# Kernel tuning notes

Hardware: AMD Instinct MI355X
Metric: run time of the kernel (lower is better)

## Reference

```python
import jax, jax.numpy as jnp
import numpy as np

B, S, H, NH = 1, 4096, 1024, 16
HD = H // NH  # head_dim = 64
ROPE_BASE = 10000.0


def setup_inputs() -> dict:
    key = jax.random.key(0)
    ks = jax.random.split(key, 8)
    sc = 0.02
    return {
        "hidden_states": jax.random.normal(ks[0], (B, S, H), jnp.float32),
        "attention_mask": jnp.zeros((B, 1, 1, S), jnp.float32),
        "Wq": jax.random.normal(ks[1], (H, H), jnp.float32) * sc,
        "bq": jnp.zeros((H,), jnp.float32),
        "Wk": jax.random.normal(ks[2], (H, H), jnp.float32) * sc,
        "bk": jnp.zeros((H,), jnp.float32),
        "Wv": jax.random.normal(ks[3], (H, H), jnp.float32) * sc,
        "bv": jnp.zeros((H,), jnp.float32),
    }


def _rope_tables(seq_len, head_dim, dtype):
    inv_freq = 1.0 / (ROPE_BASE ** (jnp.arange(0, head_dim, 2, dtype=jnp.float32) / head_dim))
    t = jnp.arange(seq_len, dtype=jnp.float32)
    freqs = jnp.einsum("s,d->sd", t, inv_freq)          # [S, HD/2]
    emb = jnp.concatenate([freqs, freqs], axis=-1)       # [S, HD]
    return jnp.cos(emb).astype(dtype), jnp.sin(emb).astype(dtype)


def _rotate_half(x):
    x1, x2 = jnp.split(x, 2, axis=-1)
    return jnp.concatenate([-x2, x1], axis=-1)


def reference(hidden_states, attention_mask, Wq, bq, Wk, bk, Wv, bv):
    bsz, q_len, _ = hidden_states.shape
    # QKV projections (torch Linear: x @ W.T + b), split into heads -> [B, NH, S, HD]
    def heads(x):
        return x.reshape(bsz, q_len, NH, HD).transpose(0, 2, 1, 3)
    q = heads(hidden_states @ Wq.T + bq)
    k = heads(hidden_states @ Wk.T + bk)
    v = heads(hidden_states @ Wv.T + bv)

    # RoPE with position_ids = arange(kv_seq_len)
    cos, sin = _rope_tables(q_len, HD, q.dtype)          # [S, HD]
    cos = cos[None, None]                                 # [1,1,S,HD]
    sin = sin[None, None]
    q = q * cos + _rotate_half(q) * sin
    k = k * cos + _rotate_half(k) * sin

    # Manual scaled-dot-product attention (baddbmm + softmax + matmul)
    scale = HD ** (-0.5)
    scores = jnp.einsum("bhqd,bhkd->bhqk", q, k) * scale  # [B,NH,S,S]
    scores = scores + attention_mask                      # broadcast additive mask
    weights = jax.nn.softmax(scores, axis=-1)
    attn = jnp.einsum("bhqk,bhkd->bhqd", weights, v)      # [B,NH,S,HD]

    # [B,S,NH,HD] -> [B,S,H]
    return attn.transpose(0, 2, 1, 3).reshape(bsz, q_len, NH * HD)
```

## Files before the change

kernel.cpp:

```cpp
#include <hip/hip_runtime.h>
#include <hip/hip_bf16.h>
#include <math.h>
#include <stdint.h>

#define S_ 4096
#define H_ 1024
#define NH_ 16
#define HD_ 64
#define LOG2E 1.4426950408889634f
#define QSCALE (0.125f * LOG2E)

typedef __bf16 bf16;
typedef __attribute__((ext_vector_type(8))) __bf16 bf16x8;
typedef __attribute__((ext_vector_type(4))) __bf16 bf16x4;
typedef __attribute__((ext_vector_type(4))) float f32x4;
typedef __attribute__((ext_vector_type(16))) float f32x16;
typedef __attribute__((ext_vector_type(2))) float f32x2;
typedef __attribute__((ext_vector_type(2))) int int2v;

__device__ __forceinline__ f32x4 mfma16(bf16x8 a, bf16x8 b, f32x4 c) {
    return __builtin_amdgcn_mfma_f32_16x16x32_bf16(a, b, c, 0, 0, 0);
}
__device__ __forceinline__ f32x16 mfma32(bf16x8 a, bf16x8 b, f32x16 c) {
    return __builtin_amdgcn_mfma_f32_32x32x16_bf16(a, b, c, 0, 0, 0);
}

__device__ __forceinline__ void gload16(const void* g, void* l) {
    __builtin_amdgcn_global_load_lds(
        (__attribute__((address_space(1))) void*)(uintptr_t)g,
        (__attribute__((address_space(3))) void*)(uintptr_t)l,
        16, 0, 0);
}

__device__ __forceinline__ unsigned cvtpk(float a, float b) {
    unsigned r;
    asm("v_cvt_pk_bf16_f32 %0, %1, %2" : "=v"(r) : "v"(a), "v"(b));
    return r;
}

__device__ __forceinline__ void swap32(unsigned a, unsigned b, unsigned& r0, unsigned& r1) {
#if __has_builtin(__builtin_amdgcn_permlane32_swap)
    int2v rr = __builtin_amdgcn_permlane32_swap((int)a, (int)b, false, false);
    r0 = (unsigned)rr[0];
    r1 = (unsigned)rr[1];
#else
    unsigned sa = (unsigned)__shfl_xor((int)a, 32, 64);
    unsigned sb = (unsigned)__shfl_xor((int)b, 32, 64);
    bool hi = (threadIdx.x & 32) != 0;
    r0 = hi ? sb : a;
    r1 = hi ? b : sa;
#endif
}

__device__ __forceinline__ float fexp2(float x) {
#if __has_builtin(__builtin_amdgcn_exp2f)
    return __builtin_amdgcn_exp2f(x);
#else
    return exp2f(x);
#endif
}

__global__ __launch_bounds__(256) void cvt_kernel(const float* __restrict__ src,
                                                  bf16* __restrict__ dst, int n) {
    int i = (blockIdx.x * 256 + threadIdx.x) * 8;
    if (i >= n) return;
    float4 v0 = *reinterpret_cast<const float4*>(src + i);
    float4 v1 = *reinterpret_cast<const float4*>(src + i + 4);
    bf16x8 o;
    o[0] = (bf16)v0.x; o[1] = (bf16)v0.y; o[2] = (bf16)v0.z; o[3] = (bf16)v0.w;
    o[4] = (bf16)v1.x; o[5] = (bf16)v1.y; o[6] = (bf16)v1.z; o[7] = (bf16)v1.w;
    *reinterpret_cast<bf16x8*>(dst + i) = o;
}

__global__ __launch_bounds__(256) void rope_table_kernel(float2* __restrict__ tab) {
    int idx = blockIdx.x * 256 + threadIdx.x;
    if (idx >= S_ * 32) return;
    int i = idx & 31, s = idx >> 5;
    double ang = (double)s * exp(-(double)(2 * i) / 64.0 * log(10000.0));
    tab[idx] = make_float2((float)cos(ang), (float)sin(ang));
}

__global__ __launch_bounds__(256) void maskl_kernel(const float* __restrict__ mask,
                                                    float* __restrict__ maskL) {
    int i = blockIdx.x * 256 + threadIdx.x;
    if (i < S_) maskL[i] = mask[i] * LOG2E;
}

__global__ __launch_bounds__(256) void qkv_gemm_kernel(
    const bf16* __restrict__ Xb,
    const bf16* __restrict__ Wqb, const bf16* __restrict__ Wkb, const bf16* __restrict__ Wvb,
    const float* __restrict__ bqp, const float* __restrict__ bkp, const float* __restrict__ bvp,
    const float2* __restrict__ tab,
    bf16* __restrict__ Qo, bf16* __restrict__ Ko, bf16* __restrict__ Vto)
{
    __shared__ bf16 Alds[128 * 64];
    __shared__ bf16 Blds[128 * 64];
    const int z = blockIdx.z;
    const bf16* W = z == 0 ? Wqb : z == 1 ? Wkb : Wvb;
    const float* bias = z == 0 ? bqp : z == 1 ? bkp : bvp;
    const int tm = blockIdx.y * 128, tn = blockIdx.x * 128;
    const int tid = threadIdx.x, lane = tid & 63, wid = tid >> 6;
    const int wm = (wid >> 1) * 64, wn = (wid & 1) * 64;
    const int lr = lane & 15, lg = lane >> 4;
    const int c_row = tid >> 3, c_sub = tid & 7;

    f32x4 acc[4][4] = {};

    for (int kt = 0; kt < H_; kt += 64) {
        #pragma unroll
        for (int is = 0; is < 4; ++is) {
            int row = is * 32 + c_row;
            int sub = c_sub ^ (row & 7);
            gload16(&Xb[(size_t)(tm + row) * H_ + kt + sub * 8],
                    &Alds[(is * 256 + wid * 64) * 8]);
            gload16(&W[(size_t)(tn + row) * H_ + kt + sub * 8],
                    &Blds[(is * 256 + wid * 64) * 8]);
        }
        __syncthreads();

        #pragma unroll
        for (int kc = 0; kc < 2; ++kc) {
            bf16x8 af[4], bfr[4];
            #pragma unroll
            for (int mb = 0; mb < 4; ++mb) {
                int row = wm + mb * 16 + lr;
                int ch = (kc * 4 + lg) ^ (row & 7);
                af[mb] = *reinterpret_cast<const bf16x8*>(&Alds[row * 64 + ch * 8]);
            }
            #pragma unroll
            for (int nb = 0; nb < 4; ++nb) {
                int row = wn + nb * 16 + lr;
                int ch = (kc * 4 + lg) ^ (row & 7);
                bfr[nb] = *reinterpret_cast<const bf16x8*>(&Blds[row * 64 + ch * 8]);
            }
            #pragma unroll
            for (int mb = 0; mb < 4; ++mb)
                #pragma unroll
                for (int nb = 0; nb < 4; ++nb)
                    acc[mb][nb] = mfma16(af[mb], bfr[nb], acc[mb][nb]);
        }
        __syncthreads();
    }

    float bv4[4];
    #pragma unroll
    for (int nb = 0; nb < 4; ++nb) bv4[nb] = bias[tn + wn + nb * 16 + lr];

    if (z < 2) {
        bf16* Y = z == 0 ? Qo : Ko;
        const float fs = z == 0 ? QSCALE : 1.0f;
        #pragma unroll
        for (int mb = 0; mb < 4; ++mb) {
            #pragma unroll
            for (int r = 0; r < 4; ++r) {
                int row = tm + wm + mb * 16 + lg * 4 + r;
                #pragma unroll
                for (int nb = 0; nb < 2; ++nb) {
                    float2 cs = tab[row * 32 + nb * 16 + lr];
                    float x1 = acc[mb][nb][r] + bv4[nb];
                    float x2 = acc[mb][nb + 2][r] + bv4[nb + 2];
                    int col = tn + wn + nb * 16 + lr;
                    Y[(size_t)row * H_ + col]      = (bf16)((x1 * cs.x - x2 * cs.y) * fs);
                    Y[(size_t)row * H_ + col + 32] = (bf16)((x2 * cs.x + x1 * cs.y) * fs);
                }
            }
        }
    } else {
        #pragma unroll
        for (int mb = 0; mb < 4; ++mb) {
            int rowb = tm + wm + mb * 16 + lg * 4;
            #pragma unroll
            for (int nb = 0; nb < 4; ++nb) {
                int col = tn + wn + nb * 16 + lr;
                bf16x4 pk;
                #pragma unroll
                for (int r = 0; r < 4; ++r) pk[r] = (bf16)(acc[mb][nb][r] + bv4[nb]);
                *reinterpret_cast<bf16x4*>(&Vto[(size_t)col * S_ + rowb]) = pk;
            }
        }
    }
}

__global__ __launch_bounds__(256) void attn_kernel(
    const bf16* __restrict__ Q, const bf16* __restrict__ K, const bf16* __restrict__ Vt,
    const float* __restrict__ maskL, float* __restrict__ out)
{
    __shared__ bf16 Kl[2][64 * 64];
    __shared__ bf16 Vl[3][64 * 64];
    const int h = blockIdx.y;
    const int qb = blockIdx.x * 128;
    const int tid = threadIdx.x, lane = tid & 63, wid = tid >> 6;
    const int l31 = lane & 31, hi = lane >> 5;
    const int srow = wid * 8 + (lane >> 3);
    const int ssub = (lane & 7) ^ (srow & 7);

    bf16x8 qf[4];
    {
        const bf16* qp = &Q[(size_t)(qb + wid * 32 + l31) * H_ + h * 64 + hi * 8];
        #pragma unroll
        for (int ks = 0; ks < 4; ++ks)
            qf[ks] = *reinterpret_cast<const bf16x8*>(qp + ks * 16);
    }

    bf16x8 vones;
    #pragma unroll
    for (int j = 0; j < 8; ++j) vones[j] = (bf16)1.0f;

    f32x16 o0 = {}, o1 = {}, lacc = {};

    const bf16* kg = &K[(size_t)srow * H_ + h * 64 + ssub * 8];
    const bf16* vg = &Vt[(size_t)(h * 64 + srow) * S_ + ssub * 8];

    auto STAGE_K = [&](int buf) {
        gload16(kg,           &Kl[buf][(wid * 8) * 64]);
        gload16(kg + 32 * H_, &Kl[buf][(32 + wid * 8) * 64]);
        kg += 64 * H_;
    };
    auto STAGE_V = [&](int buf) {
        gload16(vg,           &Vl[buf][(wid * 8) * 64]);
        gload16(vg + 32 * S_, &Vl[buf][(32 + wid * 8) * 64]);
        vg += 64;
    };

    auto QK = [&](const bf16* Kb_, const float* mrow, f32x16& q0, f32x16& q1) {
        f32x16 a, b;
        #pragma unroll
        for (int g = 0; g < 4; ++g) {
            float4 m0 = *reinterpret_cast<const float4*>(mrow + g * 8);
            a[g * 4 + 0] = m0.x; a[g * 4 + 1] = m0.y;
            a[g * 4 + 2] = m0.z; a[g * 4 + 3] = m0.w;
            float4 m1 = *reinterpret_cast<const float4*>(mrow + 32 + g * 8);
            b[g * 4 + 0] = m1.x; b[g * 4 + 1] = m1.y;
            b[g * 4 + 2] = m1.z; b[g * 4 + 3] = m1.w;
        }
        __builtin_amdgcn_s_setprio(1);
        #pragma unroll
        for (int ks = 0; ks < 4; ++ks) {
            int ch = (2 * ks + hi) ^ (l31 & 7);
            bf16x8 kf0 = *reinterpret_cast<const bf16x8*>(&Kb_[l31 * 64 + ch * 8]);
            a = mfma32(kf0, qf[ks], a);
            bf16x8 kf1 = *reinterpret_cast<const bf16x8*>(&Kb_[(32 + l31) * 64 + ch * 8]);
            b = mfma32(kf1, qf[ks], b);
        }
        __builtin_amdgcn_s_setprio(0);
        q0 = a; q1 = b;
    };

    STAGE_K(0); STAGE_V(0);
    STAGE_K(1); STAGE_V(1);
    __syncthreads();

    f32x16 scA0, scA1, scB0, scB1;
    QK(Kl[0], &maskL[hi * 4], scA0, scA1);

    int vstage = 2;
    int vread = 0;
    const float* mlp = &maskL[64 + hi * 4];
    const int NT = S_ / 64;

    auto BODY = [&](int t, f32x16& sm0, f32x16& sm1, f32x16& qk0, f32x16& qk1) {
        __syncthreads();
        if (t + 1 < NT) { QK(Kl[(t + 1) & 1], mlp, qk0, qk1); mlp += 64; }
        if (t + 2 < NT) {
            STAGE_K(t & 1);
            STAGE_V(vstage);
            vstage = vstage == 2 ? 0 : vstage + 1;
        }

        #pragma unroll
        for (int r = 0; r < 16; ++r) sm0[r] = fexp2(sm0[r]);
        #pragma unroll
        for (int r = 0; r < 16; ++r) sm1[r] = fexp2(sm1[r]);

        bf16x8 pf[4];
        #pragma unroll
        for (int ks = 0; ks < 2; ++ks) {
            unsigned w[4];
            #pragma unroll
            for (int wi = 0; wi < 2; ++wi) {
                unsigned u = cvtpk(sm0[8 * ks + 2 * wi],     sm0[8 * ks + 2 * wi + 1]);
                unsigned v = cvtpk(sm0[8 * ks + 4 + 2 * wi], sm0[8 * ks + 4 + 2 * wi + 1]);
                swap32(u, v, w[wi], w[wi + 2]);
            }
            union { unsigned u[4]; bf16x8 v; } cv;
            cv.u[0] = w[0]; cv.u[1] = w[1]; cv.u[2] = w[2]; cv.u[3] = w[3];
            pf[ks] = cv.v;
        }
        #pragma unroll
        for (int ks = 0; ks < 2; ++ks) {
            unsigned w[4];
            #pragma unroll
            for (int wi = 0; wi < 2; ++wi) {
                unsigned u = cvtpk(sm1[8 * ks + 2 * wi],     sm1[8 * ks + 2 * wi + 1]);
                unsigned v = cvtpk(sm1[8 * ks + 4 + 2 * wi], sm1[8 * ks + 4 + 2 * wi + 1]);
                swap32(u, v, w[wi], w[wi + 2]);
            }
            union { unsigned u[4]; bf16x8 v; } cv;
            cv.u[0] = w[0]; cv.u[1] = w[1]; cv.u[2] = w[2]; cv.u[3] = w[3];
            pf[2 + ks] = cv.v;
        }

        const bf16* Vb_ = Vl[vread];
        __builtin_amdgcn_s_setprio(1);
        #pragma unroll
        for (int ks = 0; ks < 4; ++ks) {
            int ch = (2 * ks + hi) ^ (l31 & 7);
            bf16x8 vf0 = *reinterpret_cast<const bf16x8*>(&Vb_[l31 * 64 + ch * 8]);
            o0 = mfma32(vf0, pf[ks], o0);
            bf16x8 vf1 = *reinterpret_cast<const bf16x8*>(&Vb_[(32 + l31) * 64 + ch * 8]);
            o1 = mfma32(vf1, pf[ks], o1);
            lacc = mfma32(vones, pf[ks], lacc);
        }
        __builtin_amdgcn_s_setprio(0);
        vread = vread == 2 ? 0 : vread + 1;
    };

    for (int t = 0; t < NT; t += 2) {
        BODY(t,     scA0, scA1, scB0, scB1);
        BODY(t + 1, scB0, scB1, scA0, scA1);
    }

    float inv = 1.f / lacc[0];
    float* orow = &out[(size_t)(qb + wid * 32 + l31) * H_ + h * 64];
    #pragma unroll
    for (int g2 = 0; g2 < 4; ++g2) {
        float4 a, b;
        a.x = o0[g2 * 4 + 0] * inv; a.y = o0[g2 * 4 + 1] * inv;
        a.z = o0[g2 * 4 + 2] * inv; a.w = o0[g2 * 4 + 3] * inv;
        b.x = o1[g2 * 4 + 0] * inv; b.y = o1[g2 * 4 + 1] * inv;
        b.z = o1[g2 * 4 + 2] * inv; b.w = o1[g2 * 4 + 3] * inv;
        *reinterpret_cast<float4*>(orow + 8 * g2 + 4 * hi) = a;
        *reinterpret_cast<float4*>(orow + 32 + 8 * g2 + 4 * hi) = b;
    }
}

extern "C" void kernel_launch(void* const* d_in, const int* in_sizes, int n_in,
                              void* d_out, int out_size, void* d_ws, size_t ws_size,
                              hipStream_t stream) {
    const float* hs   = (const float*)d_in[0];
    const float* mask = (const float*)d_in[1];
    const float* Wq   = (const float*)d_in[2];
    const float* bq   = (const float*)d_in[3];
    const float* Wk   = (const float*)d_in[4];
    const float* bk   = (const float*)d_in[5];
    const float* Wv   = (const float*)d_in[6];
    const float* bv   = (const float*)d_in[7];
    float* out = (float*)d_out;

    char* ws = (char*)d_ws;
    bf16* Xb    = (bf16*)(ws);
    bf16* Wqb   = (bf16*)(ws + (8u  << 20));
    bf16* Wkb   = (bf16*)(ws + (10u << 20));
    bf16* Wvb   = (bf16*)(ws + (12u << 20));
    bf16* Qb    = (bf16*)(ws + (14u << 20));
    bf16* Kb    = (bf16*)(ws + (22u << 20));
    bf16* Vt    = (bf16*)(ws + (30u << 20));
    float2* tab = (float2*)(ws + (38u << 20));
    float* maskL = (float*)(ws + (39u << 20));

    cvt_kernel<<<S_ * H_ / 2048, 256, 0, stream>>>(hs, Xb, S_ * H_);
    cvt_kernel<<<H_ * H_ / 2048, 256, 0, stream>>>(Wq, Wqb, H_ * H_);
    cvt_kernel<<<H_ * H_ / 2048, 256, 0, stream>>>(Wk, Wkb, H_ * H_);
    cvt_kernel<<<H_ * H_ / 2048, 256, 0, stream>>>(Wv, Wvb, H_ * H_);
    rope_table_kernel<<<(S_ * 32) / 256, 256, 0, stream>>>(tab);
    maskl_kernel<<<(S_ + 255) / 256, 256, 0, stream>>>(mask, maskL);
    qkv_gemm_kernel<<<dim3(H_ / 128, S_ / 128, 3), 256, 0, stream>>>(
        Xb, Wqb, Wkb, Wvb, bq, bk, bv, tab, Qb, Kb, Vt);
    attn_kernel<<<dim3(S_ / 128, NH_), 256, 0, stream>>>(Qb, Kb, Vt, maskL, out);
}
```

Baseline: 164.2 us.

## Fold additive mask into V and row-sum weights; merge prep launches

The additive attention mask is turned into a multiplicative weight exp(mask). That weight scales the V rows in the QKV GEMM epilogue and replaces the all-ones operand in the row-sum MFMA, so the QK accumulators start from zero instead of loading mask values every tile. The four conversion launches are merged into one kernel, and the rope-table and mask preprocessing are merged into a single prep kernel, cutting launch overhead. In exchange, the row-sum MFMA now reads a bf16 weight vector from global memory each tile. Rounding exp(mask) to bf16 can change precision, and the scheme depends on exp(mask) staying finite.

Measured after the change: 152.9 us. 1.07x faster.

```diff
diff --git a/kernel.cpp b/kernel.cpp
--- a/kernel.cpp
+++ b/kernel.cpp
@@ -60,10 +60,18 @@
 #endif
 }
 
-__global__ __launch_bounds__(256) void cvt_kernel(const float* __restrict__ src,
-                                                  bf16* __restrict__ dst, int n) {
-    int i = (blockIdx.x * 256 + threadIdx.x) * 8;
-    if (i >= n) return;
+__global__ __launch_bounds__(256) void cvt_all_kernel(
+    const float* __restrict__ hs, const float* __restrict__ Wq,
+    const float* __restrict__ Wk, const float* __restrict__ Wv,
+    bf16* __restrict__ Xb, bf16* __restrict__ Wqb,
+    bf16* __restrict__ Wkb, bf16* __restrict__ Wvb) {
+    int b = blockIdx.x;
+    const float* src; bf16* dst; size_t base;
+    if (b < 2048)      { src = hs; dst = Xb;  base = (size_t)b * 2048; }
+    else if (b < 2560) { src = Wq; dst = Wqb; base = (size_t)(b - 2048) * 2048; }
+    else if (b < 3072) { src = Wk; dst = Wkb; base = (size_t)(b - 2560) * 2048; }
+    else               { src = Wv; dst = Wvb; base = (size_t)(b - 3072) * 2048; }
+    size_t i = base + threadIdx.x * 8;
     float4 v0 = *reinterpret_cast<const float4*>(src + i);
     float4 v1 = *reinterpret_cast<const float4*>(src + i + 4);
     bf16x8 o;
@@ -72,25 +80,29 @@
     *reinterpret_cast<bf16x8*>(dst + i) = o;
 }
 
-__global__ __launch_bounds__(256) void rope_table_kernel(float2* __restrict__ tab) {
+__global__ __launch_bounds__(256) void prep_kernel(const float* __restrict__ mask,
+                                                   float2* __restrict__ tab,
+                                                   bf16* __restrict__ wM,
+                                                   float* __restrict__ wV) {
     int idx = blockIdx.x * 256 + threadIdx.x;
-    if (idx >= S_ * 32) return;
-    int i = idx & 31, s = idx >> 5;
-    double ang = (double)s * exp(-(double)(2 * i) / 64.0 * log(10000.0));
-    tab[idx] = make_float2((float)cos(ang), (float)sin(ang));
-}
-
-__global__ __launch_bounds__(256) void maskl_kernel(const float* __restrict__ mask,
-                                                    float* __restrict__ maskL) {
-    int i = blockIdx.x * 256 + threadIdx.x;
-    if (i < S_) maskL[i] = mask[i] * LOG2E;
+    if (idx < S_ * 32) {
+        int i = idx & 31, s = idx >> 5;
+        double ang = (double)s * exp(-(double)(2 * i) / 64.0 * log(10000.0));
+        tab[idx] = make_float2((float)cos(ang), (float)sin(ang));
+    }
+    if (idx < S_) {
+        float e = exp2f(mask[idx] * LOG2E);
+        bf16 eb = (bf16)e;
+        wM[idx] = eb;
+        wV[idx] = (float)eb;
+    }
 }
 
 __global__ __launch_bounds__(256) void qkv_gemm_kernel(
     const bf16* __restrict__ Xb,
     const bf16* __restrict__ Wqb, const bf16* __restrict__ Wkb, const bf16* __restrict__ Wvb,
     const float* __restrict__ bqp, const float* __restrict__ bkp, const float* __restrict__ bvp,
-    const float2* __restrict__ tab,
+    const float2* __restrict__ tab, const float* __restrict__ wV,
     bf16* __restrict__ Qo, bf16* __restrict__ Ko, bf16* __restrict__ Vto)
 {
     __shared__ bf16 Alds[128 * 64];
@@ -169,12 +181,15 @@
         #pragma unroll
         for (int mb = 0; mb < 4; ++mb) {
             int rowb = tm + wm + mb * 16 + lg * 4;
+            float4 wv = *reinterpret_cast<const float4*>(&wV[rowb]);
+            float wvr[4] = {wv.x, wv.y, wv.z, wv.w};
             #pragma unroll
             for (int nb = 0; nb < 4; ++nb) {
                 int col = tn + wn + nb * 16 + lr;
                 bf16x4 pk;
                 #pragma unroll
-                for (int r = 0; r < 4; ++r) pk[r] = (bf16)(acc[mb][nb][r] + bv4[nb]);
+                for (int r = 0; r < 4; ++r)
+                    pk[r] = (bf16)((acc[mb][nb][r] + bv4[nb]) * wvr[r]);
                 *reinterpret_cast<bf16x4*>(&Vto[(size_t)col * S_ + rowb]) = pk;
             }
         }
@@ -183,7 +198,7 @@
 
 __global__ __launch_bounds__(256) void attn_kernel(
     const bf16* __restrict__ Q, const bf16* __restrict__ K, const bf16* __restrict__ Vt,
-    const float* __restrict__ maskL, float* __restrict__ out)
+    const bf16* __restrict__ wM, float* __restrict__ out)
 {
     __shared__ bf16 Kl[2][64 * 64];
     __shared__ bf16 Vl[3][64 * 64];
@@ -201,10 +216,6 @@
         for (int ks = 0; ks < 4; ++ks)
             qf[ks] = *reinterpret_cast<const bf16x8*>(qp + ks * 16);
     }
-
-    bf16x8 vones;
-    #pragma unroll
-    for (int j = 0; j < 8; ++j) vones[j] = (bf16)1.0f;
 
     f32x16 o0 = {}, o1 = {}, lacc = {};
 
@@ -222,17 +233,8 @@
         vg += 64;
     };
 
-    auto QK = [&](const bf16* Kb_, const float* mrow, f32x16& q0, f32x16& q1) {
-        f32x16 a, b;
-        #pragma unroll
-        for (int g = 0; g < 4; ++g) {
-            float4 m0 = *reinterpret_cast<const float4*>(mrow + g * 8);
-            a[g * 4 + 0] = m0.x; a[g * 4 + 1] = m0.y;
-            a[g * 4 + 2] = m0.z; a[g * 4 + 3] = m0.w;
-            float4 m1 = *reinterpret_cast<const float4*>(mrow + 32 + g * 8);
-            b[g * 4 + 0] = m1.x; b[g * 4 + 1] = m1.y;
-            b[g * 4 + 2] = m1.z; b[g * 4 + 3] = m1.w;
-        }
+    auto QK = [&](const bf16* Kb_, f32x16& q0, f32x16& q1) {
+        f32x16 a = {}, b = {};
         __builtin_amdgcn_s_setprio(1);
         #pragma unroll
         for (int ks = 0; ks < 4; ++ks) {
@@ -251,16 +253,16 @@
     __syncthreads();
 
     f32x16 scA0, scA1, scB0, scB1;
-    QK(Kl[0], &maskL[hi * 4], scA0, scA1);
+    QK(Kl[0], scA0, scA1);
 
     int vstage = 2;
     int vread = 0;
-    const float* mlp = &maskL[64 + hi * 4];
+    const bf16* wmt = wM + hi * 8;
     const int NT = S_ / 64;
 
     auto BODY = [&](int t, f32x16& sm0, f32x16& sm1, f32x16& qk0, f32x16& qk1) {
         __syncthreads();
-        if (t + 1 < NT) { QK(Kl[(t + 1) & 1], mlp, qk0, qk1); mlp += 64; }
+        if (t + 1 < NT) QK(Kl[(t + 1) & 1], qk0, qk1);
         if (t + 2 < NT) {
             STAGE_K(t & 1);
             STAGE_V(vstage);
@@ -309,9 +311,11 @@
             o0 = mfma32(vf0, pf[ks], o0);
             bf16x8 vf1 = *reinterpret_cast<const bf16x8*>(&Vb_[(32 + l31) * 64 + ch * 8]);
             o1 = mfma32(vf1, pf[ks], o1);
-            lacc = mfma32(vones, pf[ks], lacc);
+            bf16x8 wf = *reinterpret_cast<const bf16x8*>(wmt + ks * 16);
+            lacc = mfma32(wf, pf[ks], lacc);
         }
         __builtin_amdgcn_s_setprio(0);
+        wmt += 64;
         vread = vread == 2 ? 0 : vread + 1;
     };
 
@@ -356,15 +360,12 @@
     bf16* Kb    = (bf16*)(ws + (22u << 20));
     bf16* Vt    = (bf16*)(ws + (30u << 20));
     float2* tab = (float2*)(ws + (38u << 20));
-    float* maskL = (float*)(ws + (39u << 20));
-
-    cvt_kernel<<<S_ * H_ / 2048, 256, 0, stream>>>(hs, Xb, S_ * H_);
-    cvt_kernel<<<H_ * H_ / 2048, 256, 0, stream>>>(Wq, Wqb, H_ * H_);
-    cvt_kernel<<<H_ * H_ / 2048, 256, 0, stream>>>(Wk, Wkb, H_ * H_);
-    cvt_kernel<<<H_ * H_ / 2048, 256, 0, stream>>>(Wv, Wvb, H_ * H_);
-    rope_table_kernel<<<(S_ * 32) / 256, 256, 0, stream>>>(tab);
-    maskl_kernel<<<(S_ + 255) / 256, 256, 0, stream>>>(mask, maskL);
+    bf16* wM    = (bf16*)(ws + (39u << 20));
+    float* wV   = (float*)(ws + (39u << 20) + 65536);
+
+    cvt_all_kernel<<<3584, 256, 0, stream>>>(hs, Wq, Wk, Wv, Xb, Wqb, Wkb, Wvb);
+    prep_kernel<<<(S_ * 32) / 256, 256, 0, stream>>>(mask, tab, wM, wV);
     qkv_gemm_kernel<<<dim3(H_ / 128, S_ / 128, 3), 256, 0, stream>>>(
-        Xb, Wqb, Wkb, Wvb, bq, bk, bv, tab, Qb, Kb, Vt);
-    attn_kernel<<<dim3(S_ / 128, NH_), 256, 0, stream>>>(Qb, Kb, Vt, maskL, out);
-}
+        Xb, Wqb, Wkb, Wvb, bq, bk, bv, tab, wV, Qb, Kb, Vt);
+    attn_kernel<<<dim3(S_ / 128, NH_), 256, 0, stream>>>(Qb, Kb, Vt, wM, out);
+}
```
